# Optimization experiments

Measured on AMD Instinct MI355X. Metric: run time of the kernel, lower is better.

Reference implementation:

```python
import jax, jax.numpy as jnp
import numpy as np


def _cas(N, dtype=jnp.float32):
    # cas(2*pi*k*n/N) = cos + sin, symmetric NxN matrix (rebuilt per call, as in the original)
    n = jnp.arange(N, dtype=dtype)
    ang = (2.0 * jnp.pi / N) * jnp.outer(n, n)
    return jnp.cos(ang) + jnp.sin(ang)


def dht(x):
    # Discrete Hartley transform over the last axis via dense matmul
    return x @ _cas(x.shape[-1], x.dtype)


def reverse(x):
    # X[(N - k) mod N]: index 0 stays, rest are flipped
    return jnp.roll(jnp.flip(x, axis=-1), 1, axis=-1)


def setup_inputs() -> dict:
    key = jax.random.key(0)
    k1, k2 = jax.random.split(key)
    B, Cin, Cout, N, M = 4, 16, 16, 8192, 64
    x = jax.random.normal(k1, (B, Cin, N), dtype=jnp.float32)
    scale = 1.0 / (Cin * Cout)
    weights1 = scale * jax.random.uniform(k2, (Cin, Cout, M), dtype=jnp.float32)
    return {"x": x, "weights1": weights1}


def reference(x, weights1):
    B, Cin, N = x.shape
    Cout, M = weights1.shape[1], weights1.shape[2]
    N2 = N // 2 + 1

    # DHT of the input over the spatial axis
    x_ht = dht(x)                                   # [B, Cin, N]

    # compl_mul1d on the first `modes1` Hartley coefficients
    hp = dht(x_ht[:, :, :M])                        # [B, Cin, M] (DHT applied again, as in source)
    hq = dht(weights1)                              # [Cin, Cout, M]
    rp = reverse(hp)
    rq = reverse(hq)
    # (t1 + t2 + t3 - t4)/2 == ((hp+rp)@hq + (hp-rp)@rq)/2
    hz = 0.5 * (jnp.einsum('bix,iox->box', hp + rp, hq)
                + jnp.einsum('bix,iox->box', hp - rp, rq))  # [B, Cout, M]
    # idht normalizes by the TOTAL element count of its argument (quirk preserved)
    z = dht(hz) / (B * Cout * M)                    # [B, Cout, M]

    # Scatter into half-spectrum buffer, then idht (imag part is always zero -> stay real)
    out_ht = jnp.zeros((B, Cout, N2), dtype=x.dtype).at[:, :, :M].set(z)
    out = dht(out_ht) / (B * Cout * N2)             # [B, Cout, N//2 + 1]
    return out
```

## Files before the change

### kernel.cpp

```cpp
#include <hip/hip_runtime.h>
#include <math.h>

#define TWO_PI 6.283185307179586f

__global__ __launch_bounds__(256) void k1_dht_big(const float* __restrict__ x,
                                                  float* __restrict__ P) {
  const int r  = blockIdx.x;
  const int mb = blockIdx.y;
  const int nh = blockIdx.z;
  const int t  = threadIdx.x;
  const int l  = t & 63;
  const int w  = t >> 6;
  const int mbase = mb * 32 + w * 8;
  const float* xr = x + r * 8192 + nh * 4096;

  const float step = TWO_PI / 8192.0f;
  float u[8], v[8], Cs[8], Ss[8];
  float accA[8][4];
  float accB[8][3];

#pragma unroll
  for (int q = 0; q < 8; ++q) {
    const int m = mbase + q;
    const int idx0 = ((nh * 4096 + 4 * l) * m) & 8191;
    float s0, c0;
    __sincosf((float)idx0 * step, &s0, &c0);
    u[q] = c0 + s0;
    v[q] = c0 - s0;
    const int idxs = (256 * m) & 8191;
    float ss, cs;
    __sincosf((float)idxs * step, &ss, &cs);
    Cs[q] = cs;
    Ss[q] = ss;
#pragma unroll
    for (int j = 0; j < 4; ++j) accA[q][j] = 0.0f;
#pragma unroll
    for (int j = 0; j < 3; ++j) accB[q][j] = 0.0f;
  }

#pragma unroll 4
  for (int it = 0; it < 16; ++it) {
    const float4 xv = *reinterpret_cast<const float4*>(xr + it * 256 + 4 * l);
#pragma unroll
    for (int q = 0; q < 8; ++q) {
      accA[q][0] += xv.x * u[q];
      accA[q][1] += xv.y * u[q];
      accA[q][2] += xv.z * u[q];
      accA[q][3] += xv.w * u[q];
      accB[q][0] += xv.y * v[q];
      accB[q][1] += xv.z * v[q];
      accB[q][2] += xv.w * v[q];
      const float un = Cs[q] * u[q] + Ss[q] * v[q];
      const float vn = Cs[q] * v[q] - Ss[q] * u[q];
      u[q] = un;
      v[q] = vn;
    }
  }

#pragma unroll
  for (int q = 0; q < 8; ++q) {
    const int m = mbase + q;
    const float d = (float)m * step;
    float acc = accA[q][0];
#pragma unroll
    for (int j = 1; j < 4; ++j) {
      float sj, cj;
      __sincosf((float)j * d, &sj, &cj);
      acc += cj * accA[q][j] + sj * accB[q][j - 1];
    }
#pragma unroll
    for (int off = 32; off > 0; off >>= 1) acc += __shfl_xor(acc, off, 64);
    if (l == q) P[(r * 64 + m) * 2 + nh] = acc;
  }
}

__global__ __launch_bounds__(256) void k2a_small_dht(const float* __restrict__ w1,
                                                     const float* __restrict__ P,
                                                     float* __restrict__ hp,
                                                     float* __restrict__ hq) {
  __shared__ float rows[4][64];
  __shared__ float cas64[64];
  const int t = threadIdx.x;
  const int sub = t >> 6;
  const int c = t & 63;
  if (t < 64) {
    float s, cc;
    __sincosf((float)t * (TWO_PI / 64.0f), &s, &cc);
    cas64[t] = cc + s;
  }
  const int b = blockIdx.x;
  if (b < 64) {
    rows[sub][c] = w1[(b * 4 + sub) * 64 + c];
  } else {
    const int r = (b - 64) * 4 + sub;
    rows[sub][c] = P[(r * 64 + c) * 2] + P[(r * 64 + c) * 2 + 1];
  }
  __syncthreads();
  float acc = 0.0f;
#pragma unroll 8
  for (int m = 0; m < 64; ++m) acc += rows[sub][m] * cas64[(m * c) & 63];
  if (b < 64) hq[(b * 4 + sub) * 64 + c] = acc;
  else        hp[((b - 64) * 4 + sub) * 64 + c] = acc;
}

__global__ __launch_bounds__(256) void k2b_mix(const float* __restrict__ hp,
                                               const float* __restrict__ hq,
                                               float* __restrict__ z) {
  const int blk = blockIdx.x;
  const int b = blk >> 4;
  const int o = blk & 15;
  __shared__ float shp[16][64];
  __shared__ float shq[16][64];
  __shared__ float hz[64];
  __shared__ float red[4][64];
  __shared__ float cas64[64];
  const int t = threadIdx.x;
  const int m = t & 63;
  const int sub = t >> 6;
  if (t < 64) {
    float s, cc;
    __sincosf((float)t * (TWO_PI / 64.0f), &s, &cc);
    cas64[t] = cc + s;
  }
  for (int i = sub; i < 16; i += 4) {
    shp[i][m] = hp[(b * 16 + i) * 64 + m];
    shq[i][m] = hq[(i * 16 + o) * 64 + m];
  }
  __syncthreads();
  const int mr = (64 - m) & 63;
  float a = 0.0f;
#pragma unroll
  for (int ii = 0; ii < 4; ++ii) {
    const int i = sub * 4 + ii;
    const float p  = shp[i][m];
    const float pr = shp[i][mr];
    const float qq = shq[i][m];
    const float qr = shq[i][mr];
    a += 0.5f * ((p + pr) * qq + (p - pr) * qr);
  }
  red[sub][m] = a;
  __syncthreads();
  if (t < 64) hz[t] = red[0][t] + red[1][t] + red[2][t] + red[3][t];
  __syncthreads();
  float zz = 0.0f;
#pragma unroll
  for (int j = 0; j < 16; ++j) {
    const int mm = sub * 16 + j;
    zz += hz[mm] * cas64[(mm * m) & 63];
  }
  red[sub][m] = zz;
  __syncthreads();
  if (t < 64)
    z[(b * 16 + o) * 64 + t] =
        (red[0][t] + red[1][t] + red[2][t] + red[3][t]) * (1.0f / 4096.0f);
}

__global__ __launch_bounds__(256) void k3_out(const float* __restrict__ z,
                                              float* __restrict__ out) {
  const int row = blockIdx.x;
  const int kc  = blockIdx.y;
  __shared__ float zr[64];
  const int t = threadIdx.x;
  if (t < 64) zr[t] = z[row * 64 + t];
  __syncthreads();
  const int k = kc * 256 + t;
  if (k >= 4097) return;
  const float d = (float)k * (TWO_PI / 4097.0f);
  float sd, cd;
  __sincosf(d, &sd, &cd);
  float u = 1.0f, v = 1.0f;
  float acc = 0.0f;
#pragma unroll 8
  for (int m = 0; m < 64; ++m) {
    acc += zr[m] * u;
    const float un = cd * u + sd * v;
    const float vn = cd * v - sd * u;
    u = un;
    v = vn;
  }
  out[row * 4097 + k] = acc * (1.0f / 262208.0f);
}

extern "C" void kernel_launch(void* const* d_in, const int* in_sizes, int n_in,
                              void* d_out, int out_size, void* d_ws, size_t ws_size,
                              hipStream_t stream) {
  const float* x  = (const float*)d_in[0];
  const float* w1 = (const float*)d_in[1];
  float* out = (float*)d_out;
  float* ws = (float*)d_ws;
  float* P  = ws;
  float* hp = ws + 8192;
  float* hq = ws + 12288;
  float* z  = ws + 28672;

  k1_dht_big<<<dim3(64, 2, 2), 256, 0, stream>>>(x, P);
  k2a_small_dht<<<80, 256, 0, stream>>>(w1, P, hp, hq);
  k2b_mix<<<64, 256, 0, stream>>>(hp, hq, z);
  k3_out<<<dim3(64, 17), 256, 0, stream>>>(z, out);
}
```

Before: 74.81 us.

## Merge kernels to cut launches: fold weight DHT into big DHT, hp into mix

New measurement: 74.61 us. No clear change (-0.3%).

```diff
diff --git a/kernel.cpp b/kernel.cpp
--- a/kernel.cpp
+++ b/kernel.cpp
@@ -3,160 +3,186 @@
 
 #define TWO_PI 6.283185307179586f
 
-__global__ __launch_bounds__(256) void k1_dht_big(const float* __restrict__ x,
-                                                  float* __restrict__ P) {
-  const int r  = blockIdx.x;
-  const int mb = blockIdx.y;
-  const int nh = blockIdx.z;
-  const int t  = threadIdx.x;
-  const int l  = t & 63;
-  const int w  = t >> 6;
-  const int mbase = mb * 32 + w * 8;
-  const float* xr = x + r * 8192 + nh * 4096;
-
-  const float step = TWO_PI / 8192.0f;
-  float u[8], v[8], Cs[8], Ss[8];
-  float accA[8][4];
-  float accB[8][3];
-
-#pragma unroll
-  for (int q = 0; q < 8; ++q) {
-    const int m = mbase + q;
-    const int idx0 = ((nh * 4096 + 4 * l) * m) & 8191;
-    float s0, c0;
-    __sincosf((float)idx0 * step, &s0, &c0);
-    u[q] = c0 + s0;
-    v[q] = c0 - s0;
-    const int idxs = (256 * m) & 8191;
-    float ss, cs;
-    __sincosf((float)idxs * step, &ss, &cs);
-    Cs[q] = cs;
-    Ss[q] = ss;
-#pragma unroll
-    for (int j = 0; j < 4; ++j) accA[q][j] = 0.0f;
-#pragma unroll
-    for (int j = 0; j < 3; ++j) accB[q][j] = 0.0f;
-  }
-
-#pragma unroll 4
-  for (int it = 0; it < 16; ++it) {
-    const float4 xv = *reinterpret_cast<const float4*>(xr + it * 256 + 4 * l);
-#pragma unroll
-    for (int q = 0; q < 8; ++q) {
-      accA[q][0] += xv.x * u[q];
-      accA[q][1] += xv.y * u[q];
-      accA[q][2] += xv.z * u[q];
-      accA[q][3] += xv.w * u[q];
-      accB[q][0] += xv.y * v[q];
-      accB[q][1] += xv.z * v[q];
-      accB[q][2] += xv.w * v[q];
-      const float un = Cs[q] * u[q] + Ss[q] * v[q];
-      const float vn = Cs[q] * v[q] - Ss[q] * u[q];
-      u[q] = un;
-      v[q] = vn;
-    }
-  }
-
-#pragma unroll
-  for (int q = 0; q < 8; ++q) {
-    const int m = mbase + q;
-    const float d = (float)m * step;
-    float acc = accA[q][0];
-#pragma unroll
-    for (int j = 1; j < 4; ++j) {
-      float sj, cj;
-      __sincosf((float)j * d, &sj, &cj);
-      acc += cj * accA[q][j] + sj * accB[q][j - 1];
-    }
-#pragma unroll
-    for (int off = 32; off > 0; off >>= 1) acc += __shfl_xor(acc, off, 64);
-    if (l == q) P[(r * 64 + m) * 2 + nh] = acc;
-  }
-}
-
-__global__ __launch_bounds__(256) void k2a_small_dht(const float* __restrict__ w1,
-                                                     const float* __restrict__ P,
-                                                     float* __restrict__ hp,
-                                                     float* __restrict__ hq) {
+__global__ __launch_bounds__(256) void kA(const float* __restrict__ x,
+                                          const float* __restrict__ w1,
+                                          float* __restrict__ P,
+                                          float* __restrict__ hq) {
   __shared__ float rows[4][64];
   __shared__ float cas64[64];
+  const int blk = blockIdx.x;
   const int t = threadIdx.x;
-  const int sub = t >> 6;
-  const int c = t & 63;
-  if (t < 64) {
-    float s, cc;
-    __sincosf((float)t * (TWO_PI / 64.0f), &s, &cc);
-    cas64[t] = cc + s;
-  }
-  const int b = blockIdx.x;
-  if (b < 64) {
-    rows[sub][c] = w1[(b * 4 + sub) * 64 + c];
+
+  if (blk < 256) {
+    const int r  = blk & 63;
+    const int mb = (blk >> 6) & 1;
+    const int nh = (blk >> 7) & 1;
+    const int l  = t & 63;
+    const int w  = t >> 6;
+    const int mbase = mb * 32 + w * 8;
+    const float* xr = x + r * 8192 + nh * 4096;
+
+    const float step = TWO_PI / 8192.0f;
+    float u[8], v[8], Cs[8], Ss[8];
+    float accA[8][4];
+    float accB[8][3];
+
+#pragma unroll
+    for (int q = 0; q < 8; ++q) {
+      const int m = mbase + q;
+      const int idx0 = ((nh * 4096 + 4 * l) * m) & 8191;
+      float s0, c0;
+      __sincosf((float)idx0 * step, &s0, &c0);
+      u[q] = c0 + s0;
+      v[q] = c0 - s0;
+      const int idxs = (256 * m) & 8191;
+      float ss, cs;
+      __sincosf((float)idxs * step, &ss, &cs);
+      Cs[q] = cs;
+      Ss[q] = ss;
+#pragma unroll
+      for (int j = 0; j < 4; ++j) accA[q][j] = 0.0f;
+#pragma unroll
+      for (int j = 0; j < 3; ++j) accB[q][j] = 0.0f;
+    }
+
+#pragma unroll 8
+    for (int it = 0; it < 16; ++it) {
+      const float4 xv = *reinterpret_cast<const float4*>(xr + it * 256 + 4 * l);
+#pragma unroll
+      for (int q = 0; q < 8; ++q) {
+        accA[q][0] += xv.x * u[q];
+        accA[q][1] += xv.y * u[q];
+        accA[q][2] += xv.z * u[q];
+        accA[q][3] += xv.w * u[q];
+        accB[q][0] += xv.y * v[q];
+        accB[q][1] += xv.z * v[q];
+        accB[q][2] += xv.w * v[q];
+        const float un = Cs[q] * u[q] + Ss[q] * v[q];
+        const float vn = Cs[q] * v[q] - Ss[q] * u[q];
+        u[q] = un;
+        v[q] = vn;
+      }
+    }
+
+#pragma unroll
+    for (int q = 0; q < 8; ++q) {
+      const int m = mbase + q;
+      const float d = (float)m * step;
+      float acc = accA[q][0];
+#pragma unroll
+      for (int j = 1; j < 4; ++j) {
+        float sj, cj;
+        __sincosf((float)j * d, &sj, &cj);
+        acc += cj * accA[q][j] + sj * accB[q][j - 1];
+      }
+#pragma unroll
+      for (int off = 32; off > 0; off >>= 1) acc += __shfl_xor(acc, off, 64);
+      if (l == q) P[(r * 64 + m) * 2 + nh] = acc;
+    }
   } else {
-    const int r = (b - 64) * 4 + sub;
-    rows[sub][c] = P[(r * 64 + c) * 2] + P[(r * 64 + c) * 2 + 1];
-  }
-  __syncthreads();
-  float acc = 0.0f;
-#pragma unroll 8
-  for (int m = 0; m < 64; ++m) acc += rows[sub][m] * cas64[(m * c) & 63];
-  if (b < 64) hq[(b * 4 + sub) * 64 + c] = acc;
-  else        hp[((b - 64) * 4 + sub) * 64 + c] = acc;
-}
-
-__global__ __launch_bounds__(256) void k2b_mix(const float* __restrict__ hp,
-                                               const float* __restrict__ hq,
-                                               float* __restrict__ z) {
+    const int sub = t >> 6;
+    const int c = t & 63;
+    if (t < 64) {
+      float s, cc;
+      __sincosf((float)t * (TWO_PI / 64.0f), &s, &cc);
+      cas64[t] = cc + s;
+    }
+    const int b2 = blk - 256;
+    rows[sub][c] = w1[(b2 * 4 + sub) * 64 + c];
+    __syncthreads();
+    float acc = 0.0f;
+#pragma unroll 8
+    for (int m = 0; m < 64; ++m) acc += rows[sub][m] * cas64[(m * c) & 63];
+    hq[(b2 * 4 + sub) * 64 + c] = acc;
+  }
+}
+
+__global__ __launch_bounds__(256) void kB(const float* __restrict__ P,
+                                          const float* __restrict__ hq,
+                                          float* __restrict__ z) {
   const int blk = blockIdx.x;
   const int b = blk >> 4;
   const int o = blk & 15;
-  __shared__ float shp[16][64];
-  __shared__ float shq[16][64];
+  __shared__ float sAT[64][20];
+  __shared__ float sq[16][64];
+  __shared__ float hp[16][64];
   __shared__ float hz[64];
   __shared__ float red[4][64];
   __shared__ float cas64[64];
   const int t = threadIdx.x;
   const int m = t & 63;
   const int sub = t >> 6;
+
   if (t < 64) {
     float s, cc;
     __sincosf((float)t * (TWO_PI / 64.0f), &s, &cc);
     cas64[t] = cc + s;
   }
-  for (int i = sub; i < 16; i += 4) {
-    shp[i][m] = hp[(b * 16 + i) * 64 + m];
-    shq[i][m] = hq[(i * 16 + o) * 64 + m];
-  }
-  __syncthreads();
+  for (int idx = t; idx < 1024; idx += 256) {
+    const int i = idx >> 6;
+    const int c = idx & 63;
+    const float2 pv =
+        *reinterpret_cast<const float2*>(&P[(((b * 16 + i) << 6) + c) * 2]);
+    sAT[c][i] = pv.x + pv.y;
+    sq[i][c] = hq[(((i * 16 + o) << 6)) + c];
+  }
+  __syncthreads();
+
+  {
+    float sd, cd;
+    __sincosf((float)m * (TWO_PI / 64.0f), &sd, &cd);
+    float u = 1.0f, v = 1.0f;
+    float acc0 = 0.0f, acc1 = 0.0f, acc2 = 0.0f, acc3 = 0.0f;
+#pragma unroll 8
+    for (int c = 0; c < 64; ++c) {
+      const float4 av = *reinterpret_cast<const float4*>(&sAT[c][sub * 4]);
+      acc0 += av.x * u;
+      acc1 += av.y * u;
+      acc2 += av.z * u;
+      acc3 += av.w * u;
+      const float un = cd * u + sd * v;
+      const float vn = cd * v - sd * u;
+      u = un;
+      v = vn;
+    }
+    hp[sub * 4 + 0][m] = acc0;
+    hp[sub * 4 + 1][m] = acc1;
+    hp[sub * 4 + 2][m] = acc2;
+    hp[sub * 4 + 3][m] = acc3;
+  }
+  __syncthreads();
+
   const int mr = (64 - m) & 63;
   float a = 0.0f;
 #pragma unroll
   for (int ii = 0; ii < 4; ++ii) {
     const int i = sub * 4 + ii;
-    const float p  = shp[i][m];
-    const float pr = shp[i][mr];
-    const float qq = shq[i][m];
-    const float qr = shq[i][mr];
+    const float p  = hp[i][m];
+    const float pr = hp[i][mr];
+    const float qq = sq[i][m];
+    const float qr = sq[i][mr];
     a += 0.5f * ((p + pr) * qq + (p - pr) * qr);
   }
   red[sub][m] = a;
   __syncthreads();
   if (t < 64) hz[t] = red[0][t] + red[1][t] + red[2][t] + red[3][t];
   __syncthreads();
+
   float zz = 0.0f;
 #pragma unroll
-  for (int j = 0; j < 16; ++j) {
-    const int mm = sub * 16 + j;
+  for (int jj = 0; jj < 16; ++jj) {
+    const int mm = sub * 16 + jj;
     zz += hz[mm] * cas64[(mm * m) & 63];
   }
   red[sub][m] = zz;
   __syncthreads();
   if (t < 64)
-    z[(b * 16 + o) * 64 + t] =
+    z[blk * 64 + t] =
         (red[0][t] + red[1][t] + red[2][t] + red[3][t]) * (1.0f / 4096.0f);
 }
 
-__global__ __launch_bounds__(256) void k3_out(const float* __restrict__ z,
-                                              float* __restrict__ out) {
+__global__ __launch_bounds__(256) void kC(const float* __restrict__ z,
+                                          float* __restrict__ out) {
   const int row = blockIdx.x;
   const int kc  = blockIdx.y;
   __shared__ float zr[64];
@@ -189,12 +215,10 @@
   float* out = (float*)d_out;
   float* ws = (float*)d_ws;
   float* P  = ws;
-  float* hp = ws + 8192;
-  float* hq = ws + 12288;
-  float* z  = ws + 28672;
-
-  k1_dht_big<<<dim3(64, 2, 2), 256, 0, stream>>>(x, P);
-  k2a_small_dht<<<80, 256, 0, stream>>>(w1, P, hp, hq);
-  k2b_mix<<<64, 256, 0, stream>>>(hp, hq, z);
-  k3_out<<<dim3(64, 17), 256, 0, stream>>>(z, out);
-}
+  float* hq = ws + 8192;
+  float* z  = ws + 24576;
+
+  kA<<<320, 256, 0, stream>>>(x, w1, P, hq);
+  kB<<<64, 256, 0, stream>>>(P, hq, z);
+  kC<<<dim3(64, 17), 256, 0, stream>>>(z, out);
+}
```
